# Performance work log

Hardware: AMD Instinct MI355X
Metric: run time of the kernel (lower is better)

Reference implementation:

```python
import jax, jax.numpy as jnp
import numpy as np

WS = 8            # window size (square)
NUM_HEADS = 8
DIM = 256
IMG = 256         # feature map H=W for mask construction
SHIFT = WS // 2
B = 4


def _rel_pos_index(Wh, Ww):
    coords = np.stack(np.meshgrid(np.arange(Wh), np.arange(Ww), indexing='ij'))  # (2,Wh,Ww)
    cf = coords.reshape(2, -1)
    rel = cf[:, :, None] - cf[:, None, :]        # (2,N,N)
    rel = rel.transpose(1, 2, 0).astype(np.int64)
    rel[..., 0] += Wh - 1
    rel[..., 1] += Ww - 1
    rel[..., 0] *= 2 * Ww - 1
    return rel.sum(-1)                           # (N,N)


def _shift_mask(H, W, ws, ss):
    # standard Swin shifted-window attention mask: (nW, ws*ws, ws*ws) with 0 / -100
    img = np.zeros((H, W), dtype=np.float32)
    cnt = 0
    for hs in (slice(0, -ws), slice(-ws, -ss), slice(-ss, None)):
        for wsl in (slice(0, -ws), slice(-ws, -ss), slice(-ss, None)):
            img[hs, wsl] = cnt
            cnt += 1
    m = img.reshape(H // ws, ws, W // ws, ws).transpose(0, 2, 1, 3).reshape(-1, ws * ws)
    am = m[:, None, :] - m[:, :, None]
    return np.where(am != 0, np.float32(-100.0), np.float32(0.0))


def setup_inputs() -> dict:
    key = jax.random.key(0)
    ks = jax.random.split(key, 10)
    nW = (IMG // WS) ** 2
    B_ = B * nW
    N = WS * WS
    x = jax.random.normal(ks[0], (B_, N, DIM), dtype=jnp.float32)
    y = jax.random.normal(ks[1], (B_, N, DIM), dtype=jnp.float32)
    mask = jnp.asarray(_shift_mask(IMG, IMG, WS, SHIFT))
    s = 0.02
    q_w = jax.random.normal(ks[2], (DIM, DIM), dtype=jnp.float32) * s
    q_b = jnp.zeros((DIM,), dtype=jnp.float32)
    kv_w = jax.random.normal(ks[3], (2 * DIM, DIM), dtype=jnp.float32) * s
    kv_b = jnp.zeros((2 * DIM,), dtype=jnp.float32)
    proj_w = jax.random.normal(ks[4], (DIM, DIM), dtype=jnp.float32) * s
    proj_b = jnp.zeros((DIM,), dtype=jnp.float32)
    rpb_table = jax.random.normal(ks[5], ((2 * WS - 1) ** 2, NUM_HEADS), dtype=jnp.float32) * s
    return {"x": x, "y": y, "mask": mask, "q_w": q_w, "q_b": q_b,
            "kv_w": kv_w, "kv_b": kv_b, "proj_w": proj_w, "proj_b": proj_b,
            "rpb_table": rpb_table}


def reference(x, y, mask, q_w, q_b, kv_w, kv_b, proj_w, proj_b, rpb_table):
    B_, N, C = x.shape
    H = NUM_HEADS
    hd = C // H
    scale = hd ** -0.5
    # projections
    q = (x @ q_w.T + q_b).reshape(B_, N, H, hd).transpose(0, 2, 1, 3) * scale  # (B_,H,N,hd)
    kv = (y @ kv_w.T + kv_b).reshape(B_, N, 2, H, hd)
    k = kv[:, :, 0].transpose(0, 2, 1, 3)  # (B_,H,N,hd)
    v = kv[:, :, 1].transpose(0, 2, 1, 3)
    attn = jnp.einsum('bhid,bhjd->bhij', q, k)  # (B_,H,N,N)
    # relative position bias gathered from table
    rpi = jnp.asarray(_rel_pos_index(WS, WS))           # (N,N) int
    bias = rpb_table[rpi.reshape(-1)].reshape(N, N, H).transpose(2, 0, 1)  # (H,N,N)
    attn = attn + bias[None]
    # shifted-window mask
    nW = mask.shape[0]
    attn = attn.reshape(B_ // nW, nW, H, N, N) + mask[None, :, None]
    attn = attn.reshape(B_, H, N, N)
    attn = jax.nn.softmax(attn, axis=-1)
    out = jnp.einsum('bhij,bhjd->bhid', attn, v)        # (B_,H,N,hd)
    out = out.transpose(0, 2, 1, 3).reshape(B_, N, C)
    return out @ proj_w.T + proj_b
```

## Files before the change

kernel.cpp:

```cpp
#include <hip/hip_runtime.h>

typedef _Float16 half_t;
typedef _Float16 half8  __attribute__((ext_vector_type(8)));
typedef _Float16 half4v __attribute__((ext_vector_type(4)));
typedef float    f32x4  __attribute__((ext_vector_type(4)));

#define ROWB   528
#define S_A    0
#define S_B    33792
#define SMEM_BYTES 67584
#define SCALE  0.17677669529663687f

__global__ __launch_bounds__(256) void swin_prep(
    const float* __restrict__ q_w, const float* __restrict__ kv_w,
    const float* __restrict__ proj_w, const float* __restrict__ rpb,
    const float* __restrict__ mask,
    half_t* __restrict__ w16, half_t* __restrict__ fused)
{
    int t = blockIdx.x * 256 + threadIdx.x;
    if (t < 65536)        w16[t] = (half_t)(q_w[t] * SCALE);
    else if (t < 196608)  w16[t] = (half_t)kv_w[t - 65536];
    else if (t < 262144)  w16[t] = (half_t)proj_w[t - 196608];
    else if (t < 393216) {
        int u = t - 262144;
        int cls = u >> 15, rest = u & 32767;
        int h = rest >> 12, i = (rest >> 6) & 63, j = rest & 63;
        int idx = ((i >> 3) - (j >> 3) + 7) * 15 + ((i & 7) - (j & 7) + 7);
        int wsel = (cls == 0) ? 0 : (cls == 1) ? 31 : (cls == 2) ? 992 : 1023;
        fused[u] = (half_t)(rpb[idx * 8 + h] + mask[(size_t)wsel * 4096 + i * 64 + j]);
    }
}

static __device__ __forceinline__ unsigned pk2(float a, float b) {
    union { _Float16 h[2]; unsigned u; } t;
    t.h[0] = (_Float16)a; t.h[1] = (_Float16)b; return t.u;
}

#define BUILD_FRAG(dst, P0, P1)                                          \
    do {                                                                 \
        union { unsigned u[4]; half8 h; } _u;                            \
        _Pragma("unroll")                                                \
        for (int p = 0; p < 4; ++p) {                                    \
            int _src = (p >> 1) ? srcB : srcA;                           \
            unsigned _rlo = (unsigned)__shfl((int)(P0)[p & 1], _src);    \
            unsigned _rhi = (unsigned)__shfl((int)(P1)[p & 1], _src);    \
            _u.u[p] = hi ? _rhi : _rlo;                                  \
        }                                                                \
        dst = _u.h;                                                      \
    } while (0)

__global__ __launch_bounds__(512, 2) void swin_main(
    const float* __restrict__ x, const float* __restrict__ y,
    const float* __restrict__ q_b, const float* __restrict__ kv_b,
    const float* __restrict__ proj_b,
    const half_t* __restrict__ w16, const half_t* __restrict__ fused,
    float* __restrict__ out)
{
    __shared__ __align__(16) char sm[SMEM_BYTES];
    const int tid  = threadIdx.x;
    const int w    = tid >> 6;
    const int lane = tid & 63;
    const int l15  = lane & 15;
    const int g    = lane >> 4;
    const int b    = blockIdx.x;
    const int jf0  = w * 32;
    const int srcA = ((2 * g) & 3) * 16 + l15;
    const int srcB = ((2 * g + 1) & 3) * 16 + l15;
    const int hi   = g >> 1;

    const float* xb = x + (size_t)b * 16384;
    const float* yb = y + (size_t)b * 16384;
    const half_t* wkv = w16 + 65536;

    {
        float4 fx[8], fy[8];
        #pragma unroll
        for (int it = 0; it < 4; ++it) {
            int c = tid + it * 512;
            int row = c >> 5, c8 = c & 31;
            fx[it*2+0] = *(const float4*)(xb + row * 256 + c8 * 8);
            fx[it*2+1] = *(const float4*)(xb + row * 256 + c8 * 8 + 4);
            fy[it*2+0] = *(const float4*)(yb + row * 256 + c8 * 8);
            fy[it*2+1] = *(const float4*)(yb + row * 256 + c8 * 8 + 4);
        }
        #pragma unroll
        for (int it = 0; it < 4; ++it) {
            int c = tid + it * 512;
            int row = c >> 5, c8 = c & 31;
            half8 hx, hy;
            #pragma unroll
            for (int e = 0; e < 4; ++e) {
                hx[e]   = (half_t)(&fx[it*2+0].x)[e];
                hx[e+4] = (half_t)(&fx[it*2+1].x)[e];
                hy[e]   = (half_t)(&fy[it*2+0].x)[e];
                hy[e+4] = (half_t)(&fy[it*2+1].x)[e];
            }
            int off = row * ROWB + c8 * 16;
            *(half8*)(sm + S_A + off) = hx;
            *(half8*)(sm + S_B + off) = hy;
        }
    }
    __syncthreads();

    f32x4 kacc[2][4], vacc[4][2];
    #pragma unroll
    for (int ft = 0; ft < 2; ++ft)
        #pragma unroll
        for (int tok = 0; tok < 4; ++tok) {
            f32x4 z = {0.f,0.f,0.f,0.f}; kacc[ft][tok] = z; vacc[tok][ft] = z;
        }
    #pragma unroll
    for (int kh = 0; kh < 4; ++kh) {
        half8 wbk[2][2], wbv[2][2];
        #pragma unroll
        for (int k2 = 0; k2 < 2; ++k2) {
            int k0 = (kh * 2 + k2) * 32 + g * 8;
            #pragma unroll
            for (int ft = 0; ft < 2; ++ft) {
                int jf = jf0 + ft * 16 + l15;
                wbk[k2][ft] = *(const half8*)(wkv + jf * 256 + k0);
                wbv[k2][ft] = *(const half8*)(wkv + (256 + jf) * 256 + k0);
            }
        }
        #pragma unroll
        for (int k2 = 0; k2 < 2; ++k2) {
            int k0 = (kh * 2 + k2) * 32 + g * 8;
            half8 a[4];
            #pragma unroll
            for (int tok = 0; tok < 4; ++tok)
                a[tok] = *(const half8*)(sm + S_B + (tok * 16 + l15) * ROWB + k0 * 2);
            #pragma unroll
            for (int ft = 0; ft < 2; ++ft)
                #pragma unroll
                for (int tok = 0; tok < 4; ++tok) {
                    kacc[ft][tok] = __builtin_amdgcn_mfma_f32_16x16x32_f16(wbk[k2][ft], a[tok], kacc[ft][tok], 0, 0, 0);
                    vacc[tok][ft] = __builtin_amdgcn_mfma_f32_16x16x32_f16(a[tok], wbv[k2][ft], vacc[tok][ft], 0, 0, 0);
                }
        }
    }

    unsigned kp[2][4][2], vp[4][2][2];
    #pragma unroll
    for (int ft = 0; ft < 2; ++ft) {
        float4 kb4 = *(const float4*)(kv_b + jf0 + ft * 16 + g * 4);
        #pragma unroll
        for (int tok = 0; tok < 4; ++tok) {
            kp[ft][tok][0] = pk2(kacc[ft][tok][0] + kb4.x, kacc[ft][tok][1] + kb4.y);
            kp[ft][tok][1] = pk2(kacc[ft][tok][2] + kb4.z, kacc[ft][tok][3] + kb4.w);
        }
    }
    #pragma unroll
    for (int ft = 0; ft < 2; ++ft) {
        float vb = kv_b[256 + jf0 + ft * 16 + l15];
        #pragma unroll
        for (int tok = 0; tok < 4; ++tok) {
            vp[tok][ft][0] = pk2(vacc[tok][ft][0] + vb, vacc[tok][ft][1] + vb);
            vp[tok][ft][1] = pk2(vacc[tok][ft][2] + vb, vacc[tok][ft][3] + vb);
        }
    }

    unsigned qp[2][4][2];
    {
        f32x4 qacc[2][4];
        #pragma unroll
        for (int ft = 0; ft < 2; ++ft)
            #pragma unroll
            for (int tok = 0; tok < 4; ++tok) { f32x4 z = {0.f,0.f,0.f,0.f}; qacc[ft][tok] = z; }
        #pragma unroll
        for (int kh = 0; kh < 4; ++kh) {
            half8 wbq[2][2];
            #pragma unroll
            for (int k2 = 0; k2 < 2; ++k2) {
                int k0 = (kh * 2 + k2) * 32 + g * 8;
                #pragma unroll
                for (int ft = 0; ft < 2; ++ft)
                    wbq[k2][ft] = *(const half8*)(w16 + (jf0 + ft * 16 + l15) * 256 + k0);
            }
            #pragma unroll
            for (int k2 = 0; k2 < 2; ++k2) {
                int k0 = (kh * 2 + k2) * 32 + g * 8;
                half8 a[4];
                #pragma unroll
                for (int tok = 0; tok < 4; ++tok)
                    a[tok] = *(const half8*)(sm + S_A + (tok * 16 + l15) * ROWB + k0 * 2);
                #pragma unroll
                for (int ft = 0; ft < 2; ++ft)
                    #pragma unroll
                    for (int tok = 0; tok < 4; ++tok)
                        qacc[ft][tok] = __builtin_amdgcn_mfma_f32_16x16x32_f16(wbq[k2][ft], a[tok], qacc[ft][tok], 0, 0, 0);
            }
        }
        #pragma unroll
        for (int ft = 0; ft < 2; ++ft) {
            float4 qb4 = *(const float4*)(q_b + jf0 + ft * 16 + g * 4);
            #pragma unroll
            for (int tok = 0; tok < 4; ++tok) {
                qp[ft][tok][0] = pk2(qacc[ft][tok][0] + qb4.x * SCALE, qacc[ft][tok][1] + qb4.y * SCALE);
                qp[ft][tok][1] = pk2(qacc[ft][tok][2] + qb4.z * SCALE, qacc[ft][tok][3] + qb4.w * SCALE);
            }
        }
    }

    f32x4 o[2][4];
    {
        half8 ka[4], qf[4];
        #pragma unroll
        for (int mt = 0; mt < 4; ++mt) BUILD_FRAG(ka[mt], kp[0][mt], kp[1][mt]);
        #pragma unroll
        for (int nt = 0; nt < 4; ++nt) BUILD_FRAG(qf[nt], qp[0][nt], qp[1][nt]);

        f32x4 t[4][4];
        #pragma unroll
        for (int mt = 0; mt < 4; ++mt)
            #pragma unroll
            for (int nt = 0; nt < 4; ++nt) {
                f32x4 z = {0.f,0.f,0.f,0.f};
                t[mt][nt] = __builtin_amdgcn_mfma_f32_16x16x32_f16(ka[mt], qf[nt], z, 0, 0, 0);
            }

        const int wi = b & 1023;
        const int cls = ((((wi >> 5) == 31) ? 2 : 0)) | (((wi & 31) == 31) ? 1 : 0);
        const half_t* fb = fused + ((size_t)cls * 8 + w) * 4096;
        half4v fm[4][4];
        #pragma unroll
        for (int nt = 0; nt < 4; ++nt)
            #pragma unroll
            for (int mt = 0; mt < 4; ++mt)
                fm[nt][mt] = *(const half4v*)(fb + (nt * 16 + l15) * 64 + mt * 16 + g * 4);

        #pragma unroll
        for (int nt = 0; nt < 4; ++nt) {
            #pragma unroll
            for (int mt = 0; mt < 4; ++mt)
                #pragma unroll
                for (int r = 0; r < 4; ++r)
                    t[mt][nt][r] += (float)fm[nt][mt][r];
            float m = -1e30f;
            #pragma unroll
            for (int mt = 0; mt < 4; ++mt)
                #pragma unroll
                for (int r = 0; r < 4; ++r) m = fmaxf(m, t[mt][nt][r]);
            m = fmaxf(m, __shfl_xor(m, 16));
            m = fmaxf(m, __shfl_xor(m, 32));
            float s = 0.f;
            #pragma unroll
            for (int mt = 0; mt < 4; ++mt)
                #pragma unroll
                for (int r = 0; r < 4; ++r) {
                    float p = __expf(t[mt][nt][r] - m);
                    t[mt][nt][r] = p;
                    s += p;
                }
            s += __shfl_xor(s, 16);
            s += __shfl_xor(s, 32);
            float inv = 1.f / s;
            #pragma unroll
            for (int mt = 0; mt < 4; ++mt)
                #pragma unroll
                for (int r = 0; r < 4; ++r) t[mt][nt][r] *= inv;
        }

        unsigned pp[4][4][2];
        #pragma unroll
        for (int mt = 0; mt < 4; ++mt)
            #pragma unroll
            for (int nt = 0; nt < 4; ++nt) {
                pp[mt][nt][0] = pk2(t[mt][nt][0], t[mt][nt][1]);
                pp[mt][nt][1] = pk2(t[mt][nt][2], t[mt][nt][3]);
            }

        #pragma unroll
        for (int dt = 0; dt < 2; ++dt)
            #pragma unroll
            for (int nt = 0; nt < 4; ++nt) { f32x4 z = {0.f,0.f,0.f,0.f}; o[dt][nt] = z; }
        #pragma unroll
        for (int kc = 0; kc < 2; ++kc) {
            half8 va[2], pf[4];
            #pragma unroll
            for (int dt = 0; dt < 2; ++dt) BUILD_FRAG(va[dt], vp[kc*2+0][dt], vp[kc*2+1][dt]);
            #pragma unroll
            for (int nt = 0; nt < 4; ++nt) BUILD_FRAG(pf[nt], pp[kc*2+0][nt], pp[kc*2+1][nt]);
            #pragma unroll
            for (int dt = 0; dt < 2; ++dt)
                #pragma unroll
                for (int nt = 0; nt < 4; ++nt)
                    o[dt][nt] = __builtin_amdgcn_mfma_f32_16x16x32_f16(va[dt], pf[nt], o[dt][nt], 0, 0, 0);
        }
    }

    __syncthreads();

    #pragma unroll
    for (int nt = 0; nt < 4; ++nt) {
        int i = nt * 16 + l15;
        #pragma unroll
        for (int dt = 0; dt < 2; ++dt) {
            half4v ov;
            ov[0] = (half_t)o[dt][nt][0];
            ov[1] = (half_t)o[dt][nt][1];
            ov[2] = (half_t)o[dt][nt][2];
            ov[3] = (half_t)o[dt][nt][3];
            *(half4v*)(sm + S_B + i * ROWB + (jf0 + dt * 16 + g * 4) * 2) = ov;
        }
    }
    __syncthreads();

    {
        const half_t* wp = w16 + 196608;
        f32x4 dacc[4][2];
        #pragma unroll
        for (int mt = 0; mt < 4; ++mt)
            #pragma unroll
            for (int ft = 0; ft < 2; ++ft) { f32x4 z = {0.f,0.f,0.f,0.f}; dacc[mt][ft] = z; }
        #pragma unroll
        for (int kh = 0; kh < 4; ++kh) {
            half8 wbp[2][2];
            #pragma unroll
            for (int k2 = 0; k2 < 2; ++k2) {
                int k0 = (kh * 2 + k2) * 32 + g * 8;
                #pragma unroll
                for (int ft = 0; ft < 2; ++ft)
                    wbp[k2][ft] = *(const half8*)(wp + (jf0 + ft * 16 + l15) * 256 + k0);
            }
            #pragma unroll
            for (int k2 = 0; k2 < 2; ++k2) {
                int k0 = (kh * 2 + k2) * 32 + g * 8;
                half8 a[4];
                #pragma unroll
                for (int mt = 0; mt < 4; ++mt)
                    a[mt] = *(const half8*)(sm + S_B + (mt * 16 + l15) * ROWB + k0 * 2);
                #pragma unroll
                for (int mt = 0; mt < 4; ++mt)
                    #pragma unroll
                    for (int ft = 0; ft < 2; ++ft)
                        dacc[mt][ft] = __builtin_amdgcn_mfma_f32_16x16x32_f16(wbp[k2][ft], a[mt], dacc[mt][ft], 0, 0, 0);
            }
        }
        float* ob = out + (size_t)b * 16384;
        #pragma unroll
        for (int ft = 0; ft < 2; ++ft) {
            float4 pb4 = *(const float4*)(proj_b + jf0 + ft * 16 + g * 4);
            #pragma unroll
            for (int mt = 0; mt < 4; ++mt) {
                float4 v;
                v.x = dacc[mt][ft][0] + pb4.x;
                v.y = dacc[mt][ft][1] + pb4.y;
                v.z = dacc[mt][ft][2] + pb4.z;
                v.w = dacc[mt][ft][3] + pb4.w;
                *(float4*)(ob + (mt * 16 + l15) * 256 + jf0 + ft * 16 + g * 4) = v;
            }
        }
    }
}

extern "C" void kernel_launch(void* const* d_in, const int* in_sizes, int n_in,
                              void* d_out, int out_size, void* d_ws, size_t ws_size,
                              hipStream_t stream) {
    const float* x      = (const float*)d_in[0];
    const float* y      = (const float*)d_in[1];
    const float* mask   = (const float*)d_in[2];
    const float* q_w    = (const float*)d_in[3];
    const float* q_b    = (const float*)d_in[4];
    const float* kv_w   = (const float*)d_in[5];
    const float* kv_b   = (const float*)d_in[6];
    const float* proj_w = (const float*)d_in[7];
    const float* proj_b = (const float*)d_in[8];
    const float* rpb    = (const float*)d_in[9];

    half_t* w16   = (half_t*)d_ws;
    half_t* fused = (half_t*)((char*)d_ws + 524288);

    swin_prep<<<1536, 256, 0, stream>>>(q_w, kv_w, proj_w, rpb, mask, w16, fused);
    swin_main<<<4096, 512, 0, stream>>>(x, y, q_b, kv_b, proj_b,
                                        w16, fused, (float*)d_out);
}
```

Before: 469.4 us.

## Load x/y fragments directly from global, shrink LDS to fragment-ordered O buffer

Drops the LDS staging of the fp32 x and y tiles. Each wave now loads and converts its MFMA A-fragments straight from global memory. The attention output is written to a smaller LDS buffer in MFMA fragment order using shuffle-built fragments, and the bias/mask table is pre-permuted into fragment order for contiguous per-lane loads. This cuts LDS use from about 66KB to 32KB and removes one barrier, at the cost of every wave re-reading x/y rows from global/L2 (8x redundant traffic per block).

```diff
diff --git a/kernel.cpp b/kernel.cpp
--- a/kernel.cpp
+++ b/kernel.cpp
@@ -5,17 +5,13 @@
 typedef _Float16 half4v __attribute__((ext_vector_type(4)));
 typedef float    f32x4  __attribute__((ext_vector_type(4)));
 
-#define ROWB   528
-#define S_A    0
-#define S_B    33792
-#define SMEM_BYTES 67584
 #define SCALE  0.17677669529663687f
 
 __global__ __launch_bounds__(256) void swin_prep(
     const float* __restrict__ q_w, const float* __restrict__ kv_w,
     const float* __restrict__ proj_w, const float* __restrict__ rpb,
     const float* __restrict__ mask,
-    half_t* __restrict__ w16, half_t* __restrict__ fused)
+    half_t* __restrict__ w16, half_t* __restrict__ fusedF)
 {
     int t = blockIdx.x * 256 + threadIdx.x;
     if (t < 65536)        w16[t] = (half_t)(q_w[t] * SCALE);
@@ -23,17 +19,26 @@
     else if (t < 262144)  w16[t] = (half_t)proj_w[t - 196608];
     else if (t < 393216) {
         int u = t - 262144;
-        int cls = u >> 15, rest = u & 32767;
-        int h = rest >> 12, i = (rest >> 6) & 63, j = rest & 63;
+        int cls = u >> 15, q = u & 32767;
+        int h = q >> 12, s = q & 4095;
+        int nt = s >> 10, mt = (s >> 8) & 3, lane = (s >> 2) & 63, r = s & 3;
+        int g = lane >> 4, l15 = lane & 15;
+        int i = nt * 16 + l15, j = mt * 16 + g * 4 + r;
         int idx = ((i >> 3) - (j >> 3) + 7) * 15 + ((i & 7) - (j & 7) + 7);
         int wsel = (cls == 0) ? 0 : (cls == 1) ? 31 : (cls == 2) ? 992 : 1023;
-        fused[u] = (half_t)(rpb[idx * 8 + h] + mask[(size_t)wsel * 4096 + i * 64 + j]);
+        fusedF[u] = (half_t)(rpb[idx * 8 + h] + mask[(size_t)wsel * 4096 + i * 64 + j]);
     }
 }
 
 static __device__ __forceinline__ unsigned pk2(float a, float b) {
     union { _Float16 h[2]; unsigned u; } t;
     t.h[0] = (_Float16)a; t.h[1] = (_Float16)b; return t.u;
+}
+static __device__ __forceinline__ half8 cvt8(float4 a, float4 b) {
+    half8 h;
+    h[0] = (half_t)a.x; h[1] = (half_t)a.y; h[2] = (half_t)a.z; h[3] = (half_t)a.w;
+    h[4] = (half_t)b.x; h[5] = (half_t)b.y; h[6] = (half_t)b.z; h[7] = (half_t)b.w;
+    return h;
 }
 
 #define BUILD_FRAG(dst, P0, P1)                                          \
@@ -49,14 +54,14 @@
         dst = _u.h;                                                      \
     } while (0)
 
-__global__ __launch_bounds__(512, 2) void swin_main(
+__global__ __launch_bounds__(512, 2) void swin_fused(
     const float* __restrict__ x, const float* __restrict__ y,
     const float* __restrict__ q_b, const float* __restrict__ kv_b,
     const float* __restrict__ proj_b,
-    const half_t* __restrict__ w16, const half_t* __restrict__ fused,
+    const half_t* __restrict__ w16, const half_t* __restrict__ fusedF,
     float* __restrict__ out)
 {
-    __shared__ __align__(16) char sm[SMEM_BYTES];
+    __shared__ __align__(16) half_t Osm[16384];
     const int tid  = threadIdx.x;
     const int w    = tid >> 6;
     const int lane = tid & 63;
@@ -67,40 +72,11 @@
     const int srcA = ((2 * g) & 3) * 16 + l15;
     const int srcB = ((2 * g + 1) & 3) * 16 + l15;
     const int hi   = g >> 1;
+    const half_t* wkv = w16 + 65536;
+    const half_t* wpj = w16 + 196608;
 
     const float* xb = x + (size_t)b * 16384;
     const float* yb = y + (size_t)b * 16384;
-    const half_t* wkv = w16 + 65536;
-
-    {
-        float4 fx[8], fy[8];
-        #pragma unroll
-        for (int it = 0; it < 4; ++it) {
-            int c = tid + it * 512;
-            int row = c >> 5, c8 = c & 31;
-            fx[it*2+0] = *(const float4*)(xb + row * 256 + c8 * 8);
-            fx[it*2+1] = *(const float4*)(xb + row * 256 + c8 * 8 + 4);
-            fy[it*2+0] = *(const float4*)(yb + row * 256 + c8 * 8);
-            fy[it*2+1] = *(const float4*)(yb + row * 256 + c8 * 8 + 4);
-        }
-        #pragma unroll
-        for (int it = 0; it < 4; ++it) {
-            int c = tid + it * 512;
-            int row = c >> 5, c8 = c & 31;
-            half8 hx, hy;
-            #pragma unroll
-            for (int e = 0; e < 4; ++e) {
-                hx[e]   = (half_t)(&fx[it*2+0].x)[e];
-                hx[e+4] = (half_t)(&fx[it*2+1].x)[e];
-                hy[e]   = (half_t)(&fy[it*2+0].x)[e];
-                hy[e+4] = (half_t)(&fy[it*2+1].x)[e];
-            }
-            int off = row * ROWB + c8 * 16;
-            *(half8*)(sm + S_A + off) = hx;
-            *(half8*)(sm + S_B + off) = hy;
-        }
-    }
-    __syncthreads();
 
     f32x4 kacc[2][4], vacc[4][2];
     #pragma unroll
@@ -110,50 +86,37 @@
             f32x4 z = {0.f,0.f,0.f,0.f}; kacc[ft][tok] = z; vacc[tok][ft] = z;
         }
     #pragma unroll
-    for (int kh = 0; kh < 4; ++kh) {
-        half8 wbk[2][2], wbv[2][2];
-        #pragma unroll
-        for (int k2 = 0; k2 < 2; ++k2) {
-            int k0 = (kh * 2 + k2) * 32 + g * 8;
-            #pragma unroll
-            for (int ft = 0; ft < 2; ++ft) {
-                int jf = jf0 + ft * 16 + l15;
-                wbk[k2][ft] = *(const half8*)(wkv + jf * 256 + k0);
-                wbv[k2][ft] = *(const half8*)(wkv + (256 + jf) * 256 + k0);
-            }
-        }
-        #pragma unroll
-        for (int k2 = 0; k2 < 2; ++k2) {
-            int k0 = (kh * 2 + k2) * 32 + g * 8;
-            half8 a[4];
-            #pragma unroll
-            for (int tok = 0; tok < 4; ++tok)
-                a[tok] = *(const half8*)(sm + S_B + (tok * 16 + l15) * ROWB + k0 * 2);
-            #pragma unroll
-            for (int ft = 0; ft < 2; ++ft)
-                #pragma unroll
-                for (int tok = 0; tok < 4; ++tok) {
-                    kacc[ft][tok] = __builtin_amdgcn_mfma_f32_16x16x32_f16(wbk[k2][ft], a[tok], kacc[ft][tok], 0, 0, 0);
-                    vacc[tok][ft] = __builtin_amdgcn_mfma_f32_16x16x32_f16(a[tok], wbv[k2][ft], vacc[tok][ft], 0, 0, 0);
-                }
-        }
-    }
-
+    for (int kh = 0; kh < 8; ++kh) {
+        int k0 = kh * 32 + g * 8;
+        half8 wk[2], wv[2], a[4];
+        #pragma unroll
+        for (int ft = 0; ft < 2; ++ft) {
+            int jf = jf0 + ft * 16 + l15;
+            wk[ft] = *(const half8*)(wkv + jf * 256 + k0);
+            wv[ft] = *(const half8*)(wkv + (256 + jf) * 256 + k0);
+        }
+        #pragma unroll
+        for (int tok = 0; tok < 4; ++tok) {
+            const float* s = yb + (tok * 16 + l15) * 256 + k0;
+            a[tok] = cvt8(*(const float4*)s, *(const float4*)(s + 4));
+        }
+        #pragma unroll
+        for (int ft = 0; ft < 2; ++ft)
+            #pragma unroll
+            for (int tok = 0; tok < 4; ++tok) {
+                kacc[ft][tok] = __builtin_amdgcn_mfma_f32_16x16x32_f16(wk[ft], a[tok], kacc[ft][tok], 0, 0, 0);
+                vacc[tok][ft] = __builtin_amdgcn_mfma_f32_16x16x32_f16(a[tok], wv[ft], vacc[tok][ft], 0, 0, 0);
+            }
+    }
     unsigned kp[2][4][2], vp[4][2][2];
     #pragma unroll
     for (int ft = 0; ft < 2; ++ft) {
         float4 kb4 = *(const float4*)(kv_b + jf0 + ft * 16 + g * 4);
+        float  vb  = kv_b[256 + jf0 + ft * 16 + l15];
         #pragma unroll
         for (int tok = 0; tok < 4; ++tok) {
             kp[ft][tok][0] = pk2(kacc[ft][tok][0] + kb4.x, kacc[ft][tok][1] + kb4.y);
             kp[ft][tok][1] = pk2(kacc[ft][tok][2] + kb4.z, kacc[ft][tok][3] + kb4.w);
-        }
-    }
-    #pragma unroll
-    for (int ft = 0; ft < 2; ++ft) {
-        float vb = kv_b[256 + jf0 + ft * 16 + l15];
-        #pragma unroll
-        for (int tok = 0; tok < 4; ++tok) {
             vp[tok][ft][0] = pk2(vacc[tok][ft][0] + vb, vacc[tok][ft][1] + vb);
             vp[tok][ft][1] = pk2(vacc[tok][ft][2] + vb, vacc[tok][ft][3] + vb);
         }
@@ -167,36 +130,30 @@
             #pragma unroll
             for (int tok = 0; tok < 4; ++tok) { f32x4 z = {0.f,0.f,0.f,0.f}; qacc[ft][tok] = z; }
         #pragma unroll
-        for (int kh = 0; kh < 4; ++kh) {
-            half8 wbq[2][2];
-            #pragma unroll
-            for (int k2 = 0; k2 < 2; ++k2) {
-                int k0 = (kh * 2 + k2) * 32 + g * 8;
-                #pragma unroll
-                for (int ft = 0; ft < 2; ++ft)
-                    wbq[k2][ft] = *(const half8*)(w16 + (jf0 + ft * 16 + l15) * 256 + k0);
-            }
-            #pragma unroll
-            for (int k2 = 0; k2 < 2; ++k2) {
-                int k0 = (kh * 2 + k2) * 32 + g * 8;
-                half8 a[4];
+        for (int kh = 0; kh < 8; ++kh) {
+            int k0 = kh * 32 + g * 8;
+            half8 wq[2], a[4];
+            #pragma unroll
+            for (int ft = 0; ft < 2; ++ft)
+                wq[ft] = *(const half8*)(w16 + (jf0 + ft * 16 + l15) * 256 + k0);
+            #pragma unroll
+            for (int tok = 0; tok < 4; ++tok) {
+                const float* s = xb + (tok * 16 + l15) * 256 + k0;
+                a[tok] = cvt8(*(const float4*)s, *(const float4*)(s + 4));
+            }
+            #pragma unroll
+            for (int ft = 0; ft < 2; ++ft)
                 #pragma unroll
                 for (int tok = 0; tok < 4; ++tok)
-                    a[tok] = *(const half8*)(sm + S_A + (tok * 16 + l15) * ROWB + k0 * 2);
-                #pragma unroll
-                for (int ft = 0; ft < 2; ++ft)
-                    #pragma unroll
-                    for (int tok = 0; tok < 4; ++tok)
-                        qacc[ft][tok] = __builtin_amdgcn_mfma_f32_16x16x32_f16(wbq[k2][ft], a[tok], qacc[ft][tok], 0, 0, 0);
-            }
+                    qacc[ft][tok] = __builtin_amdgcn_mfma_f32_16x16x32_f16(wq[ft], a[tok], qacc[ft][tok], 0, 0, 0);
         }
         #pragma unroll
         for (int ft = 0; ft < 2; ++ft) {
-            float4 qb4 = *(const float4*)(q_b + jf0 + ft * 16 + g * 4);
+            float4 q4 = *(const float4*)(q_b + jf0 + ft * 16 + g * 4);
             #pragma unroll
             for (int tok = 0; tok < 4; ++tok) {
-                qp[ft][tok][0] = pk2(qacc[ft][tok][0] + qb4.x * SCALE, qacc[ft][tok][1] + qb4.y * SCALE);
-                qp[ft][tok][1] = pk2(qacc[ft][tok][2] + qb4.z * SCALE, qacc[ft][tok][3] + qb4.w * SCALE);
+                qp[ft][tok][0] = pk2(qacc[ft][tok][0] + q4.x * SCALE, qacc[ft][tok][1] + q4.y * SCALE);
+                qp[ft][tok][1] = pk2(qacc[ft][tok][2] + q4.z * SCALE, qacc[ft][tok][3] + q4.w * SCALE);
             }
         }
     }
@@ -220,13 +177,13 @@
 
         const int wi = b & 1023;
         const int cls = ((((wi >> 5) == 31) ? 2 : 0)) | (((wi & 31) == 31) ? 1 : 0);
-        const half_t* fb = fused + ((size_t)cls * 8 + w) * 4096;
+        const half_t* fb = fusedF + ((size_t)cls * 8 + w) * 4096;
         half4v fm[4][4];
         #pragma unroll
         for (int nt = 0; nt < 4; ++nt)
             #pragma unroll
             for (int mt = 0; mt < 4; ++mt)
-                fm[nt][mt] = *(const half4v*)(fb + (nt * 16 + l15) * 64 + mt * 16 + g * 4);
+                fm[nt][mt] = *(const half4v*)(fb + (nt * 4 + mt) * 256 + lane * 4);
 
         #pragma unroll
         for (int nt = 0; nt < 4; ++nt) {
@@ -288,53 +245,45 @@
         }
     }
 
+    {
+        unsigned po[2][4][2];
+        #pragma unroll
+        for (int dt = 0; dt < 2; ++dt)
+            #pragma unroll
+            for (int nt = 0; nt < 4; ++nt) {
+                po[dt][nt][0] = pk2(o[dt][nt][0], o[dt][nt][1]);
+                po[dt][nt][1] = pk2(o[dt][nt][2], o[dt][nt][3]);
+            }
+        #pragma unroll
+        for (int nt = 0; nt < 4; ++nt) {
+            half8 f;
+            BUILD_FRAG(f, po[0][nt], po[1][nt]);
+            *(half8*)(Osm + (w * 4 + nt) * 512 + lane * 8) = f;
+        }
+    }
     __syncthreads();
 
-    #pragma unroll
-    for (int nt = 0; nt < 4; ++nt) {
-        int i = nt * 16 + l15;
-        #pragma unroll
-        for (int dt = 0; dt < 2; ++dt) {
-            half4v ov;
-            ov[0] = (half_t)o[dt][nt][0];
-            ov[1] = (half_t)o[dt][nt][1];
-            ov[2] = (half_t)o[dt][nt][2];
-            ov[3] = (half_t)o[dt][nt][3];
-            *(half4v*)(sm + S_B + i * ROWB + (jf0 + dt * 16 + g * 4) * 2) = ov;
-        }
-    }
-    __syncthreads();
-
     {
-        const half_t* wp = w16 + 196608;
         f32x4 dacc[4][2];
         #pragma unroll
         for (int mt = 0; mt < 4; ++mt)
             #pragma unroll
             for (int ft = 0; ft < 2; ++ft) { f32x4 z = {0.f,0.f,0.f,0.f}; dacc[mt][ft] = z; }
         #pragma unroll
-        for (int kh = 0; kh < 4; ++kh) {
-            half8 wbp[2][2];
-            #pragma unroll
-            for (int k2 = 0; k2 < 2; ++k2) {
-                int k0 = (kh * 2 + k2) * 32 + g * 8;
+        for (int hc = 0; hc < 8; ++hc) {
+            int k0 = hc * 32 + g * 8;
+            half8 wbp[2], a[4];
+            #pragma unroll
+            for (int ft = 0; ft < 2; ++ft)
+                wbp[ft] = *(const half8*)(wpj + (jf0 + ft * 16 + l15) * 256 + k0);
+            #pragma unroll
+            for (int mt = 0; mt < 4; ++mt)
+                a[mt] = *(const half8*)(Osm + (hc * 4 + mt) * 512 + lane * 8);
+            #pragma unroll
+            for (int mt = 0; mt < 4; ++mt)
                 #pragma unroll
                 for (int ft = 0; ft < 2; ++ft)
-                    wbp[k2][ft] = *(const half8*)(wp + (jf0 + ft * 16 + l15) * 256 + k0);
-            }
-            #pragma unroll
-            for (int k2 = 0; k2 < 2; ++k2) {
-                int k0 = (kh * 2 + k2) * 32 + g * 8;
-                half8 a[4];
-                #pragma unroll
-                for (int mt = 0; mt < 4; ++mt)
-                    a[mt] = *(const half8*)(sm + S_B + (mt * 16 + l15) * ROWB + k0 * 2);
-                #pragma unroll
-                for (int mt = 0; mt < 4; ++mt)
-                    #pragma unroll
-                    for (int ft = 0; ft < 2; ++ft)
-                        dacc[mt][ft] = __builtin_amdgcn_mfma_f32_16x16x32_f16(wbp[k2][ft], a[mt], dacc[mt][ft], 0, 0, 0);
-            }
+                    dacc[mt][ft] = __builtin_amdgcn_mfma_f32_16x16x32_f16(wbp[ft], a[mt], dacc[mt][ft], 0, 0, 0);
         }
         float* ob = out + (size_t)b * 16384;
         #pragma unroll
@@ -342,12 +291,12 @@
             float4 pb4 = *(const float4*)(proj_b + jf0 + ft * 16 + g * 4);
             #pragma unroll
             for (int mt = 0; mt < 4; ++mt) {
-                float4 v;
-                v.x = dacc[mt][ft][0] + pb4.x;
-                v.y = dacc[mt][ft][1] + pb4.y;
-                v.z = dacc[mt][ft][2] + pb4.z;
-                v.w = dacc[mt][ft][3] + pb4.w;
-                *(float4*)(ob + (mt * 16 + l15) * 256 + jf0 + ft * 16 + g * 4) = v;
+                f32x4 v;
+                v[0] = dacc[mt][ft][0] + pb4.x;
+                v[1] = dacc[mt][ft][1] + pb4.y;
+                v[2] = dacc[mt][ft][2] + pb4.z;
+                v[3] = dacc[mt][ft][3] + pb4.w;
+                *(f32x4*)(ob + (mt * 16 + l15) * 256 + jf0 + ft * 16 + g * 4) = v;
             }
         }
     }
@@ -366,11 +315,11 @@
     const float* proj_w = (const float*)d_in[7];
     const float* proj_b = (const float*)d_in[8];
     const float* rpb    = (const float*)d_in[9];
-
-    half_t* w16   = (half_t*)d_ws;
-    half_t* fused = (half_t*)((char*)d_ws + 524288);
-
-    swin_prep<<<1536, 256, 0, stream>>>(q_w, kv_w, proj_w, rpb, mask, w16, fused);
-    swin_main<<<4096, 512, 0, stream>>>(x, y, q_b, kv_b, proj_b,
-                                        w16, fused, (float*)d_out);
-}
+    float* out          = (float*)d_out;
+
+    half_t* w16    = (half_t*)d_ws;
+    half_t* fusedF = (half_t*)((char*)d_ws + 524288);
+
+    swin_prep<<<1536, 256, 0, stream>>>(q_w, kv_w, proj_w, rpb, mask, w16, fusedF);
+    swin_fused<<<4096, 512, 0, stream>>>(x, y, q_b, kv_b, proj_b, w16, fusedF, out);
+}
```

New measurement: 1.057 ms. +125.2%, slower.
